# Kernel optimization log

Measured on AMD Instinct MI355X. Metric: run time of the kernel, lower is better.

Reference implementation:

```python
import jax, jax.numpy as jnp
import numpy as np

N = 50000
E = 400000
IN_DIM = 256
HEADS = 4
C = 64          # out_channels per head
HC = HEADS * C  # 256
OUT_DIM = 32
NEG_SLOPE = 0.2


def setup_inputs() -> dict:
    key = jax.random.key(0)
    ks = jax.random.split(key, 16)
    s = lambda fan_in: 1.0 / np.sqrt(fan_in)
    return {
        "x": jax.random.normal(ks[0], (N, IN_DIM), jnp.float32),
        "edge_index": jax.random.randint(ks[1], (2, E), 0, N, jnp.int64),
        # conv1 (lin_l == lin_r, shared)
        "W1": jax.random.normal(ks[2], (IN_DIM, HC), jnp.float32) * s(IN_DIM),
        "b1": jnp.zeros((HC,), jnp.float32),
        "att1": jax.random.normal(ks[3], (HEADS, C), jnp.float32) * s(C),
        # conv2
        "W2": jax.random.normal(ks[4], (HC, HC), jnp.float32) * s(HC),
        "b2": jnp.zeros((HC,), jnp.float32),
        "att2": jax.random.normal(ks[5], (HEADS, C), jnp.float32) * s(C),
        # post_mp: Linear(HC, C_hidden=64) -> Linear(64, OUT_DIM)
        "Wp1": jax.random.normal(ks[6], (HC, C), jnp.float32) * s(HC),
        "bp1": jnp.zeros((C,), jnp.float32),
        "Wp2": jax.random.normal(ks[7], (C, OUT_DIM), jnp.float32) * s(C),
        "bp2": jnp.zeros((OUT_DIM,), jnp.float32),
    }


def _gatv2_layer(x, src, dst, W, b, att):
    # shared lin_l == lin_r, so x_source == x_target projection
    h = (x @ W + b).reshape(-1, HEADS, C)          # [N, H, C]
    x_j = h[src]                                    # source features per edge [E, H, C]
    x_i = h[dst]                                    # target features per edge [E, H, C]
    e = jax.nn.leaky_relu(x_i + x_j, NEG_SLOPE)     # [E, H, C]
    alpha = jnp.einsum('ehc,hc->eh', e, att)        # [E, H]
    # segment softmax grouped by target node (dst)
    amax = jax.ops.segment_max(alpha, dst, num_segments=N)   # [N, H]
    ex = jnp.exp(alpha - amax[dst])
    denom = jax.ops.segment_sum(ex, dst, num_segments=N)     # [N, H]
    alpha = ex / (denom[dst] + 1e-16)
    out = jax.ops.segment_sum(x_j * alpha[:, :, None], dst, num_segments=N)  # [N, H, C]
    return out.reshape(-1, HC)


def reference(x, edge_index, W1, b1, att1, W2, b2, att2, Wp1, bp1, Wp2, bp2):
    src, dst = edge_index[0], edge_index[1]
    h = jax.nn.relu(_gatv2_layer(x, src, dst, W1, b1, att1))
    h = jax.nn.relu(_gatv2_layer(h, src, dst, W2, b2, att2))
    out = (h @ Wp1 + bp1) @ Wp2 + bp2
    return jax.nn.sigmoid(out)
```

## Files before the change

### kernel.cpp

```cpp
#include <hip/hip_runtime.h>
#include <math.h>

#define HC 256
#define NEG_SLOPE 0.2f

typedef __attribute__((ext_vector_type(2))) _Float16 h16x2;
typedef __attribute__((ext_vector_type(4))) _Float16 h16x4;
typedef __attribute__((ext_vector_type(8))) _Float16 f16x8;
typedef __attribute__((ext_vector_type(4))) float f32x4;

__device__ __forceinline__ unsigned short f2h16(float f) {
  _Float16 x = (_Float16)f;
  return __builtin_bit_cast(unsigned short, x);
}
__device__ __forceinline__ float h2f(unsigned short u) {
  _Float16 x = __builtin_bit_cast(_Float16, u);
  return (float)x;
}

__device__ __forceinline__ int detect64(const int* e) {
  int v = e[2 * (threadIdx.x & 63) + 1];
  return (__ballot(v != 0) == 0ULL) ? 1 : 0;
}

__device__ __forceinline__ int edge_val(const void* p, int is64, long long idx) {
  return is64 ? (int)((const long long*)p)[idx] : ((const int*)p)[idx];
}

__device__ __forceinline__ int wave_incl_scan(int v) {
  int lane = threadIdx.x & 63;
#pragma unroll
  for (int off = 1; off < 64; off <<= 1) {
    int y = __shfl_up(v, off, 64);
    if (lane >= off) v += y;
  }
  return v;
}

__global__ __launch_bounds__(256) void count_prep_kernel(
    const void* __restrict__ edges, int* __restrict__ counts, int E, int CB,
    const float* __restrict__ W1, const float* __restrict__ W2,
    const float* __restrict__ Wp1, const float* __restrict__ bp1,
    const float* __restrict__ Wp2, const float* __restrict__ bp2,
    unsigned short* __restrict__ W1t, unsigned short* __restrict__ W2t,
    unsigned short* __restrict__ Wft16, float* __restrict__ bf) {
  const int b = blockIdx.x, t = threadIdx.x;
  if (b < CB) {
    int is64 = detect64((const int*)edges);
    int e = b * 256 + t;
    if (e < E) {
      int dst = edge_val(edges, is64, (long long)E + e);
      atomicAdd(&counts[dst], 1);
    }
    return;
  }
  const int pb = b - CB;
  if (pb < 512) {
    int n = pb & 255;
    const float* W = (pb >> 8) ? W2 : W1;
    unsigned short* Wt = (pb >> 8) ? W2t : W1t;
    Wt[(size_t)n * 256 + t] = f2h16(W[(size_t)t * 256 + n]);
    return;
  }
  float acc[32];
#pragma unroll
  for (int o = 0; o < 32; ++o) acc[o] = 0.f;
  for (int ll = 0; ll < 64; ++ll) {
    float w1 = Wp1[t * 64 + ll];
#pragma unroll
    for (int o = 0; o < 32; ++o) acc[o] += w1 * Wp2[ll * 32 + o];
  }
#pragma unroll
  for (int o = 0; o < 32; ++o) Wft16[o * 256 + t] = f2h16(acc[o]);
  if (t < 32) {
    float s = bp2[t];
    for (int ll = 0; ll < 64; ++ll) s += bp1[ll] * Wp2[ll * 32 + t];
    bf[t] = s;
  }
}

__global__ __launch_bounds__(1024) void scan1_kernel(const int* __restrict__ counts,
                                                     int* __restrict__ excl,
                                                     int* __restrict__ partials, int N) {
  __shared__ int wsum[16];
  int i = blockIdx.x * 1024 + threadIdx.x;
  int wid = threadIdx.x >> 6, lane = threadIdx.x & 63;
  int v = (i < N) ? counts[i] : 0;
  int incl = wave_incl_scan(v);
  if (lane == 63) wsum[wid] = incl;
  __syncthreads();
  if (wid == 0) {
    int s = (lane < 16) ? wsum[lane] : 0;
    s = wave_incl_scan(s);
    if (lane < 16) wsum[lane] = s;
  }
  __syncthreads();
  int base = (wid > 0) ? wsum[wid - 1] : 0;
  if (i < N) excl[i] = base + incl - v;
  if (threadIdx.x == 1023) partials[blockIdx.x] = base + incl;
}

__global__ void scan2_kernel(int* __restrict__ partials, int P) {
  int lane = threadIdx.x;
  if (P <= 64) {
    int v = (lane < P) ? partials[lane] : 0;
    int incl = wave_incl_scan(v);
    if (lane < P) partials[lane] = incl - v;
  } else if (lane == 0) {
    int run = 0;
    for (int i = 0; i < P; ++i) { int v = partials[i]; partials[i] = run; run += v; }
  }
}

__global__ void scan3copy_kernel(int* __restrict__ excl, const int* __restrict__ partials,
                                 int* __restrict__ cursor, int N, int E) {
  int i = blockIdx.x * blockDim.x + threadIdx.x;
  if (i < N) {
    int v = excl[i] + partials[i >> 10];
    excl[i] = v;
    cursor[i] = v;
  }
  if (i == 0) excl[N] = E;
}

template <bool AF32>
__device__ __forceinline__ void gemm_body(
    const void* __restrict__ Araw, const unsigned short* __restrict__ Bt,
    const float* __restrict__ bias, unsigned short* __restrict__ C, int M,
    int orig, int nwg) {
  __shared__ __align__(16) short As[2][128 * 64];
  __shared__ __align__(16) short Bs[2][128 * 64];
  const int q = nwg >> 3, r = nwg & 7;
  const int xcd = orig & 7, pos = orig >> 3;
  const int logical = (xcd < r ? xcd * (q + 1) : r * (q + 1) + (xcd - r) * q) + pos;
  const int m0 = (logical >> 1) * 128, n0 = (logical & 1) * 128;

  const int t = threadIdx.x;
  const int l = t & 63, w = t >> 6;
  const int wr = w >> 1, wc = w & 1;
  const int l15 = l & 15, lg = l >> 4;

  const int ccs = ((t & 7) ^ ((t >> 3) & 7)) * 8;
  int rowL[4], ldsI[4];
#pragma unroll
  for (int i = 0; i < 4; ++i) {
    rowL[i] = i * 32 + (t >> 3);
    ldsI[i] = (i * 256 + t) * 8;
  }

  f32x4 acc[4][4];
#pragma unroll
  for (int m = 0; m < 4; ++m)
#pragma unroll
    for (int n = 0; n < 4; ++n) acc[m][n] = (f32x4){0.f, 0.f, 0.f, 0.f};

  uint4 ra[4], rb[4];
  auto LOAD = [&](int ks) {
    int k0 = ks * 64;
#pragma unroll
    for (int i = 0; i < 4; ++i) {
      int ar = m0 + rowL[i];
      ar = (ar < M) ? ar : (M - 1);
      if (AF32) {
        const float* A = (const float*)Araw;
        float4 fa = *(const float4*)(A + (size_t)ar * 256 + k0 + ccs);
        float4 fb = *(const float4*)(A + (size_t)ar * 256 + k0 + ccs + 4);
        ra[i].x = f2h16(fa.x) | ((unsigned)f2h16(fa.y) << 16);
        ra[i].y = f2h16(fa.z) | ((unsigned)f2h16(fa.w) << 16);
        ra[i].z = f2h16(fb.x) | ((unsigned)f2h16(fb.y) << 16);
        ra[i].w = f2h16(fb.z) | ((unsigned)f2h16(fb.w) << 16);
      } else {
        const unsigned short* A = (const unsigned short*)Araw;
        ra[i] = *(const uint4*)(A + (size_t)ar * 256 + k0 + ccs);
      }
      rb[i] = *(const uint4*)(Bt + (size_t)(n0 + rowL[i]) * 256 + k0 + ccs);
    }
  };
  auto WRITE = [&](int buf) {
#pragma unroll
    for (int i = 0; i < 4; ++i) {
      *(uint4*)&As[buf][ldsI[i]] = ra[i];
      *(uint4*)&Bs[buf][ldsI[i]] = rb[i];
    }
  };

  int rA[4], rB[4];
#pragma unroll
  for (int m = 0; m < 4; ++m) rA[m] = (wr * 64 + m * 16 + l15) * 64;
#pragma unroll
  for (int n = 0; n < 4; ++n) rB[n] = (wc * 64 + n * 16 + l15) * 64;
  const int swz0 = ((0 * 4 + lg) ^ (l & 7)) * 8;
  const int swz1 = ((1 * 4 + lg) ^ (l & 7)) * 8;

  LOAD(0);
  WRITE(0);
  __syncthreads();
  for (int ks = 0; ks < 4; ++ks) {
    if (ks < 3) LOAD(ks + 1);
    const int buf = ks & 1;
#pragma unroll
    for (int kk = 0; kk < 2; ++kk) {
      const int swz = kk ? swz1 : swz0;
      f16x8 a[4], b[4];
#pragma unroll
      for (int m = 0; m < 4; ++m) a[m] = *(const f16x8*)&As[buf][rA[m] + swz];
#pragma unroll
      for (int n = 0; n < 4; ++n) b[n] = *(const f16x8*)&Bs[buf][rB[n] + swz];
#pragma unroll
      for (int m = 0; m < 4; ++m)
#pragma unroll
        for (int n = 0; n < 4; ++n)
          acc[m][n] = __builtin_amdgcn_mfma_f32_16x16x32_f16(a[m], b[n], acc[m][n], 0, 0, 0);
    }
    if (ks < 3) WRITE((ks + 1) & 1);
    __syncthreads();
  }

  float bcol[4];
#pragma unroll
  for (int n = 0; n < 4; ++n) bcol[n] = bias[n0 + wc * 64 + n * 16 + l15];
#pragma unroll
  for (int m = 0; m < 4; ++m) {
    int baseRow = m0 + wr * 64 + m * 16 + lg * 4;
#pragma unroll
    for (int rr = 0; rr < 4; ++rr) {
      int row = baseRow + rr;
      if (row < M) {
#pragma unroll
        for (int n = 0; n < 4; ++n)
          C[(size_t)row * 256 + n0 + wc * 64 + n * 16 + l15] = f2h16(acc[m][n][rr] + bcol[n]);
      }
    }
  }
}

__global__ __launch_bounds__(256) void gemm1_fill_kernel(
    const float* __restrict__ x, const unsigned short* __restrict__ W1t,
    const float* __restrict__ b1, unsigned short* __restrict__ h, int M, int GB,
    const void* __restrict__ edges, int* __restrict__ cursor,
    int* __restrict__ csr_src, int E) {
  if ((int)blockIdx.x < GB) {
    gemm_body<true>((const void*)x, W1t, b1, h, M, blockIdx.x, GB);
    return;
  }
  int is64 = detect64((const int*)edges);
  int e = (blockIdx.x - GB) * 256 + threadIdx.x;
  if (e >= E) return;
  int src = edge_val(edges, is64, e);
  int dst = edge_val(edges, is64, (long long)E + e);
  int p = atomicAdd(&cursor[dst], 1);
  csr_src[p] = src;
}

__global__ __launch_bounds__(256) void gemm2_kernel(
    const unsigned short* __restrict__ A, const unsigned short* __restrict__ W2t,
    const float* __restrict__ b2, unsigned short* __restrict__ h, int M) {
  gemm_body<false>((const void*)A, W2t, b2, h, M, blockIdx.x, gridDim.x);
}

__global__ __launch_bounds__(256) void gat_fused_kernel(
    const unsigned short* __restrict__ h, const float* __restrict__ att,
    const int* __restrict__ row_ptr, const int* __restrict__ csr_src,
    unsigned short* __restrict__ out16, int N) {
  const int wid = threadIdx.x >> 6, ln = threadIdx.x & 63;
  const int node = blockIdx.x * 4 + wid;
  if (node >= N) return;
  const float4 attv = *(const float4*)(att + ln * 4);
  const h16x4 at4 = {(_Float16)attv.x, (_Float16)attv.y, (_Float16)attv.z, (_Float16)attv.w};
  const _Float16 kns = (_Float16)NEG_SLOPE;
  const h16x4 k4 = {kns, kns, kns, kns};
  const h16x4 hi4 = *(const h16x4*)(h + (size_t)node * HC + ln * 4);
  const int beg = __builtin_amdgcn_readfirstlane(row_ptr[node]);
  const int end = __builtin_amdgcn_readfirstlane(row_ptr[node + 1]);
  const size_t vo = (size_t)ln * 4;

  float d = 0.f;
  float4 S = make_float4(0.f, 0.f, 0.f, 0.f);

  int e0 = beg;
  for (; e0 + 8 <= end; e0 += 8) {
    h16x4 hj[8];
    float p[8];
#pragma unroll
    for (int c = 0; c < 8; ++c) {
      int j = __builtin_amdgcn_readfirstlane(csr_src[e0 + c]);
      hj[c] = *(const h16x4*)(h + (size_t)j * HC + vo);
    }
#pragma unroll
    for (int c = 0; c < 8; ++c) {
      h16x4 s4 = hi4 + hj[c];
      h16x4 l4 = __builtin_elementwise_max(s4, s4 * k4);
      h16x4 m4 = l4 * at4;
      h16x2 a2 = m4.lo + m4.hi;
      float pp = (float)a2.x + (float)a2.y;
#pragma unroll
      for (int off = 1; off < 16; off <<= 1) pp += __shfl_xor(pp, off, 64);
      p[c] = pp;
    }
#pragma unroll
    for (int c = 0; c < 8; ++c) {
      float wgt = __expf(p[c]);
      d += wgt;
      S.x += wgt * (float)hj[c].x;
      S.y += wgt * (float)hj[c].y;
      S.z += wgt * (float)hj[c].z;
      S.w += wgt * (float)hj[c].w;
    }
  }
  if (e0 < end) {
    const int cnt = end - e0;
    h16x4 hj[8];
    float p[8];
#pragma unroll
    for (int c = 0; c < 8; ++c) {
      int j = __builtin_amdgcn_readfirstlane(csr_src[min(e0 + c, end - 1)]);
      hj[c] = *(const h16x4*)(h + (size_t)j * HC + vo);
    }
#pragma unroll
    for (int c = 0; c < 8; ++c) {
      h16x4 s4 = hi4 + hj[c];
      h16x4 l4 = __builtin_elementwise_max(s4, s4 * k4);
      h16x4 m4 = l4 * at4;
      h16x2 a2 = m4.lo + m4.hi;
      float pp = (float)a2.x + (float)a2.y;
#pragma unroll
      for (int off = 1; off < 16; off <<= 1) pp += __shfl_xor(pp, off, 64);
      p[c] = pp;
    }
#pragma unroll
    for (int c = 0; c < 8; ++c) {
      float wgt = (c < cnt) ? __expf(p[c]) : 0.f;
      d += wgt;
      S.x += wgt * (float)hj[c].x;
      S.y += wgt * (float)hj[c].y;
      S.z += wgt * (float)hj[c].z;
      S.w += wgt * (float)hj[c].w;
    }
  }

  float inv = (d > 0.f) ? (1.f / d) : 0.f;
  ushort4 ub;
  ub.x = f2h16(fmaxf(S.x * inv, 0.f));
  ub.y = f2h16(fmaxf(S.y * inv, 0.f));
  ub.z = f2h16(fmaxf(S.z * inv, 0.f));
  ub.w = f2h16(fmaxf(S.w * inv, 0.f));
  *(ushort4*)(out16 + (size_t)node * HC + vo) = ub;
}

__global__ __launch_bounds__(256) void post_kernel(
    const unsigned short* __restrict__ g, const unsigned short* __restrict__ Wft16,
    const float* __restrict__ bf, float* __restrict__ out, int M) {
  const int l = threadIdx.x & 63, w = threadIdx.x >> 6;
  const int r0 = blockIdx.x * 256 + w * 64;
  const int l15 = l & 15, lg = l >> 4;

  f16x8 bfrag[2][8];
#pragma unroll
  for (int n = 0; n < 2; ++n)
#pragma unroll
    for (int ks = 0; ks < 8; ++ks)
      bfrag[n][ks] = *(const f16x8*)(Wft16 + (size_t)(n * 16 + l15) * 256 + ks * 32 + lg * 8);

  float b0 = bf[l15], b1 = bf[16 + l15];

  f32x4 acc[4][2];
#pragma unroll
  for (int m = 0; m < 4; ++m)
#pragma unroll
    for (int n = 0; n < 2; ++n) acc[m][n] = (f32x4){0.f, 0.f, 0.f, 0.f};

#pragma unroll
  for (int m = 0; m < 4; ++m) {
    int row = r0 + m * 16 + l15;
    row = (row < M) ? row : (M - 1);
    const unsigned short* gp = g + (size_t)row * 256 + lg * 8;
#pragma unroll
    for (int ks = 0; ks < 8; ++ks) {
      f16x8 a = *(const f16x8*)(gp + ks * 32);
      acc[m][0] = __builtin_amdgcn_mfma_f32_16x16x32_f16(a, bfrag[0][ks], acc[m][0], 0, 0, 0);
      acc[m][1] = __builtin_amdgcn_mfma_f32_16x16x32_f16(a, bfrag[1][ks], acc[m][1], 0, 0, 0);
    }
  }

#pragma unroll
  for (int m = 0; m < 4; ++m) {
    int baseRow = r0 + m * 16 + lg * 4;
#pragma unroll
    for (int rr = 0; rr < 4; ++rr) {
      int row = baseRow + rr;
      if (row < M) {
        float v0 = acc[m][0][rr] + b0;
        float v1 = acc[m][1][rr] + b1;
        out[(size_t)row * 32 + l15]      = 1.f / (1.f + __expf(-v0));
        out[(size_t)row * 32 + 16 + l15] = 1.f / (1.f + __expf(-v1));
      }
    }
  }
}

extern "C" void kernel_launch(void* const* d_in, const int* in_sizes, int n_in,
                              void* d_out, int out_size, void* d_ws, size_t ws_size,
                              hipStream_t stream) {
  const float* x    = (const float*)d_in[0];
  const void*  ei   = d_in[1];
  const float* W1   = (const float*)d_in[2];
  const float* b1   = (const float*)d_in[3];
  const float* att1 = (const float*)d_in[4];
  const float* W2   = (const float*)d_in[5];
  const float* b2   = (const float*)d_in[6];
  const float* att2 = (const float*)d_in[7];
  const float* Wp1  = (const float*)d_in[8];
  const float* bp1  = (const float*)d_in[9];
  const float* Wp2  = (const float*)d_in[10];
  const float* bp2  = (const float*)d_in[11];
  const int N = in_sizes[0] / 256;
  const int E = in_sizes[1] / 2;
  float* outp = (float*)d_out;

  char* ws = (char*)d_ws;
  size_t off = 0;
  auto alloc = [&](size_t bytes) {
    char* p = ws + off;
    off = (off + bytes + 255) & ~(size_t)255;
    return p;
  };
  unsigned short* h16  = (unsigned short*)alloc((size_t)N * 256 * 2);
  unsigned short* a16  = (unsigned short*)alloc((size_t)N * 256 * 2);
  unsigned short* g16  = (unsigned short*)alloc((size_t)N * 256 * 2);
  int*   row_ptr  = (int*)alloc((size_t)(N + 1) * 4);
  int*   cursor   = (int*)alloc((size_t)N * 4);
  int*   csr      = (int*)alloc((size_t)E * 4);
  int*   partials = (int*)alloc((size_t)((N + 1023) / 1024 + 1) * 4);
  unsigned short* W1t = (unsigned short*)alloc(256 * 256 * 2);
  unsigned short* W2t = (unsigned short*)alloc(256 * 256 * 2);
  unsigned short* Wft16 = (unsigned short*)alloc(32 * 256 * 2);
  float* bfv      = (float*)alloc(32 * 4);

  const int nb = (N + 255) / 256;
  const int eb = (E + 255) / 256;
  const int P  = (N + 1023) / 1024;
  const int mt = (N + 127) / 128;
  const int GB = mt * 2;

  hipMemsetAsync(cursor, 0, (size_t)N * 4, stream);
  hipLaunchKernelGGL(count_prep_kernel, dim3(eb + 513), dim3(256), 0, stream,
                     ei, cursor, E, eb, W1, W2, Wp1, bp1, Wp2, bp2, W1t, W2t, Wft16, bfv);
  hipLaunchKernelGGL(scan1_kernel, dim3(P), dim3(1024), 0, stream, cursor, row_ptr, partials, N);
  hipLaunchKernelGGL(scan2_kernel, dim3(1), dim3(64), 0, stream, partials, P);
  hipLaunchKernelGGL(scan3copy_kernel, dim3(nb), dim3(256), 0, stream, row_ptr, partials, cursor, N, E);
  hipLaunchKernelGGL(gemm1_fill_kernel, dim3(GB + eb), dim3(256), 0, stream,
                     x, W1t, b1, h16, N, GB, ei, cursor, csr, E);
  hipLaunchKernelGGL(gat_fused_kernel, dim3((N + 3) / 4), dim3(256), 0, stream,
                     h16, att1, row_ptr, csr, a16, N);
  hipLaunchKernelGGL(gemm2_kernel, dim3(GB), dim3(256), 0, stream, a16, W2t, b2, h16, N);
  hipLaunchKernelGGL(gat_fused_kernel, dim3((N + 3) / 4), dim3(256), 0, stream,
                     h16, att2, row_ptr, csr, g16, N);
  hipLaunchKernelGGL(post_kernel, dim3((N + 255) / 256), dim3(256), 0, stream,
                     g16, Wft16, bfv, outp, N);
}
```

Before: 190.1 us.

## Stream A from global with full-K B tile in LDS; use fdot2 for attention

The GEMM is restructured so each block loads a 64-column by full-K slice of the transposed weight into LDS once. It then streams A rows straight from global memory into MFMA registers, with each wave covering 64 rows and the block covering 256 rows. This removes the double-buffered A/B LDS pipeline and its per-step barriers, at the cost of A being read four times (once per column block) and having no software prefetch. Separately, the attention logit computation in the GAT kernel switches from half-precision multiply and adds to fdot2 with fp32 accumulation.

```diff
diff --git a/kernel.cpp b/kernel.cpp
--- a/kernel.cpp
+++ b/kernel.cpp
@@ -124,28 +124,37 @@
 }
 
 template <bool AF32>
-__device__ __forceinline__ void gemm_body(
+__device__ __forceinline__ void gemm_stream(
     const void* __restrict__ Araw, const unsigned short* __restrict__ Bt,
     const float* __restrict__ bias, unsigned short* __restrict__ C, int M,
     int orig, int nwg) {
-  __shared__ __align__(16) short As[2][128 * 64];
-  __shared__ __align__(16) short Bs[2][128 * 64];
+  __shared__ __align__(16) short Bs[64 * 256];
   const int q = nwg >> 3, r = nwg & 7;
   const int xcd = orig & 7, pos = orig >> 3;
   const int logical = (xcd < r ? xcd * (q + 1) : r * (q + 1) + (xcd - r) * q) + pos;
-  const int m0 = (logical >> 1) * 128, n0 = (logical & 1) * 128;
+  const int mb = (logical >> 2) * 256, n0 = (logical & 3) * 64;
 
   const int t = threadIdx.x;
   const int l = t & 63, w = t >> 6;
-  const int wr = w >> 1, wc = w & 1;
   const int l15 = l & 15, lg = l >> 4;
 
-  const int ccs = ((t & 7) ^ ((t >> 3) & 7)) * 8;
-  int rowL[4], ldsI[4];
-#pragma unroll
-  for (int i = 0; i < 4; ++i) {
-    rowL[i] = i * 32 + (t >> 3);
-    ldsI[i] = (i * 256 + t) * 8;
+  {
+    const int row = t >> 2, qtr = t & 3;
+    const unsigned short* src = Bt + (size_t)(n0 + row) * 256;
+#pragma unroll
+    for (int i = 0; i < 8; ++i) {
+      int c = qtr * 8 + i;
+      uint4 v = *(const uint4*)(src + c * 8);
+      *(uint4*)&Bs[row * 256 + ((c ^ (row & 7)) * 8)] = v;
+    }
+  }
+  __syncthreads();
+
+  int arow[4];
+#pragma unroll
+  for (int m = 0; m < 4; ++m) {
+    int rr = mb + w * 64 + m * 16 + l15;
+    arow[m] = (rr < M) ? rr : (M - 1);
   }
 
   f32x4 acc[4][4];
@@ -154,81 +163,53 @@
 #pragma unroll
     for (int n = 0; n < 4; ++n) acc[m][n] = (f32x4){0.f, 0.f, 0.f, 0.f};
 
-  uint4 ra[4], rb[4];
-  auto LOAD = [&](int ks) {
-    int k0 = ks * 64;
-#pragma unroll
-    for (int i = 0; i < 4; ++i) {
-      int ar = m0 + rowL[i];
-      ar = (ar < M) ? ar : (M - 1);
+  int bbase[4], brow7[4];
+#pragma unroll
+  for (int n = 0; n < 4; ++n) {
+    int row = n * 16 + l15;
+    bbase[n] = row * 256;
+    brow7[n] = row & 7;
+  }
+
+#pragma unroll
+  for (int ks = 0; ks < 8; ++ks) {
+    f16x8 bfr[4];
+#pragma unroll
+    for (int n = 0; n < 4; ++n) {
+      int c = ks * 4 + lg;
+      bfr[n] = *(const f16x8*)&Bs[bbase[n] + ((c ^ brow7[n]) * 8)];
+    }
+#pragma unroll
+    for (int m = 0; m < 4; ++m) {
+      f16x8 a;
       if (AF32) {
-        const float* A = (const float*)Araw;
-        float4 fa = *(const float4*)(A + (size_t)ar * 256 + k0 + ccs);
-        float4 fb = *(const float4*)(A + (size_t)ar * 256 + k0 + ccs + 4);
-        ra[i].x = f2h16(fa.x) | ((unsigned)f2h16(fa.y) << 16);
-        ra[i].y = f2h16(fa.z) | ((unsigned)f2h16(fa.w) << 16);
-        ra[i].z = f2h16(fb.x) | ((unsigned)f2h16(fb.y) << 16);
-        ra[i].w = f2h16(fb.z) | ((unsigned)f2h16(fb.w) << 16);
+        const float* A = (const float*)Araw + (size_t)arow[m] * 256 + ks * 32 + lg * 8;
+        float4 fa = *(const float4*)(A);
+        float4 fb = *(const float4*)(A + 4);
+        a[0] = (_Float16)fa.x; a[1] = (_Float16)fa.y; a[2] = (_Float16)fa.z; a[3] = (_Float16)fa.w;
+        a[4] = (_Float16)fb.x; a[5] = (_Float16)fb.y; a[6] = (_Float16)fb.z; a[7] = (_Float16)fb.w;
       } else {
-        const unsigned short* A = (const unsigned short*)Araw;
-        ra[i] = *(const uint4*)(A + (size_t)ar * 256 + k0 + ccs);
+        a = *(const f16x8*)((const unsigned short*)Araw + (size_t)arow[m] * 256 + ks * 32 + lg * 8);
       }
-      rb[i] = *(const uint4*)(Bt + (size_t)(n0 + rowL[i]) * 256 + k0 + ccs);
-    }
-  };
-  auto WRITE = [&](int buf) {
-#pragma unroll
-    for (int i = 0; i < 4; ++i) {
-      *(uint4*)&As[buf][ldsI[i]] = ra[i];
-      *(uint4*)&Bs[buf][ldsI[i]] = rb[i];
-    }
-  };
-
-  int rA[4], rB[4];
-#pragma unroll
-  for (int m = 0; m < 4; ++m) rA[m] = (wr * 64 + m * 16 + l15) * 64;
-#pragma unroll
-  for (int n = 0; n < 4; ++n) rB[n] = (wc * 64 + n * 16 + l15) * 64;
-  const int swz0 = ((0 * 4 + lg) ^ (l & 7)) * 8;
-  const int swz1 = ((1 * 4 + lg) ^ (l & 7)) * 8;
-
-  LOAD(0);
-  WRITE(0);
-  __syncthreads();
-  for (int ks = 0; ks < 4; ++ks) {
-    if (ks < 3) LOAD(ks + 1);
-    const int buf = ks & 1;
-#pragma unroll
-    for (int kk = 0; kk < 2; ++kk) {
-      const int swz = kk ? swz1 : swz0;
-      f16x8 a[4], b[4];
-#pragma unroll
-      for (int m = 0; m < 4; ++m) a[m] = *(const f16x8*)&As[buf][rA[m] + swz];
-#pragma unroll
-      for (int n = 0; n < 4; ++n) b[n] = *(const f16x8*)&Bs[buf][rB[n] + swz];
-#pragma unroll
-      for (int m = 0; m < 4; ++m)
-#pragma unroll
-        for (int n = 0; n < 4; ++n)
-          acc[m][n] = __builtin_amdgcn_mfma_f32_16x16x32_f16(a[m], b[n], acc[m][n], 0, 0, 0);
-    }
-    if (ks < 3) WRITE((ks + 1) & 1);
-    __syncthreads();
+#pragma unroll
+      for (int n = 0; n < 4; ++n)
+        acc[m][n] = __builtin_amdgcn_mfma_f32_16x16x32_f16(a, bfr[n], acc[m][n], 0, 0, 0);
+    }
   }
 
   float bcol[4];
 #pragma unroll
-  for (int n = 0; n < 4; ++n) bcol[n] = bias[n0 + wc * 64 + n * 16 + l15];
+  for (int n = 0; n < 4; ++n) bcol[n] = bias[n0 + n * 16 + l15];
 #pragma unroll
   for (int m = 0; m < 4; ++m) {
-    int baseRow = m0 + wr * 64 + m * 16 + lg * 4;
+    int baseRow = mb + w * 64 + m * 16 + lg * 4;
 #pragma unroll
     for (int rr = 0; rr < 4; ++rr) {
       int row = baseRow + rr;
       if (row < M) {
 #pragma unroll
         for (int n = 0; n < 4; ++n)
-          C[(size_t)row * 256 + n0 + wc * 64 + n * 16 + l15] = f2h16(acc[m][n][rr] + bcol[n]);
+          C[(size_t)row * 256 + n0 + n * 16 + l15] = f2h16(acc[m][n][rr] + bcol[n]);
       }
     }
   }
@@ -240,7 +221,7 @@
     const void* __restrict__ edges, int* __restrict__ cursor,
     int* __restrict__ csr_src, int E) {
   if ((int)blockIdx.x < GB) {
-    gemm_body<true>((const void*)x, W1t, b1, h, M, blockIdx.x, GB);
+    gemm_stream<true>((const void*)x, W1t, b1, h, M, blockIdx.x, GB);
     return;
   }
   int is64 = detect64((const int*)edges);
@@ -255,7 +236,7 @@
 __global__ __launch_bounds__(256) void gemm2_kernel(
     const unsigned short* __restrict__ A, const unsigned short* __restrict__ W2t,
     const float* __restrict__ b2, unsigned short* __restrict__ h, int M) {
-  gemm_body<false>((const void*)A, W2t, b2, h, M, blockIdx.x, gridDim.x);
+  gemm_stream<false>((const void*)A, W2t, b2, h, M, blockIdx.x, gridDim.x);
 }
 
 __global__ __launch_bounds__(256) void gat_fused_kernel(
@@ -266,7 +247,8 @@
   const int node = blockIdx.x * 4 + wid;
   if (node >= N) return;
   const float4 attv = *(const float4*)(att + ln * 4);
-  const h16x4 at4 = {(_Float16)attv.x, (_Float16)attv.y, (_Float16)attv.z, (_Float16)attv.w};
+  const h16x2 at_lo = {(_Float16)attv.x, (_Float16)attv.y};
+  const h16x2 at_hi = {(_Float16)attv.z, (_Float16)attv.w};
   const _Float16 kns = (_Float16)NEG_SLOPE;
   const h16x4 k4 = {kns, kns, kns, kns};
   const h16x4 hi4 = *(const h16x4*)(h + (size_t)node * HC + ln * 4);
@@ -290,9 +272,8 @@
     for (int c = 0; c < 8; ++c) {
       h16x4 s4 = hi4 + hj[c];
       h16x4 l4 = __builtin_elementwise_max(s4, s4 * k4);
-      h16x4 m4 = l4 * at4;
-      h16x2 a2 = m4.lo + m4.hi;
-      float pp = (float)a2.x + (float)a2.y;
+      float pp = __builtin_amdgcn_fdot2(l4.lo, at_lo,
+                 __builtin_amdgcn_fdot2(l4.hi, at_hi, 0.f, false), false);
 #pragma unroll
       for (int off = 1; off < 16; off <<= 1) pp += __shfl_xor(pp, off, 64);
       p[c] = pp;
@@ -320,9 +301,8 @@
     for (int c = 0; c < 8; ++c) {
       h16x4 s4 = hi4 + hj[c];
       h16x4 l4 = __builtin_elementwise_max(s4, s4 * k4);
-      h16x4 m4 = l4 * at4;
-      h16x2 a2 = m4.lo + m4.hi;
-      float pp = (float)a2.x + (float)a2.y;
+      float pp = __builtin_amdgcn_fdot2(l4.lo, at_lo,
+                 __builtin_amdgcn_fdot2(l4.hi, at_hi, 0.f, false), false);
 #pragma unroll
       for (int off = 1; off < 16; off <<= 1) pp += __shfl_xor(pp, off, 64);
       p[c] = pp;
@@ -439,8 +419,7 @@
   const int nb = (N + 255) / 256;
   const int eb = (E + 255) / 256;
   const int P  = (N + 1023) / 1024;
-  const int mt = (N + 127) / 128;
-  const int GB = mt * 2;
+  const int GB = ((N + 255) / 256) * 4;
 
   hipMemsetAsync(cursor, 0, (size_t)N * 4, stream);
   hipLaunchKernelGGL(count_prep_kernel, dim3(eb + 513), dim3(256), 0, stream,
```

After: 232.1 us. 1.22x slower.
